# Kernel tuning notes

Measured on AMD Instinct MI355X. Metric: run time of the kernel, lower is better.

The kernel has to match this reference:

```python
import jax, jax.numpy as jnp
import numpy as np

N_NODES = 100000
N_EDGES = 3200000
D = 128


def setup_inputs() -> dict:
    key = jax.random.key(0)
    k1, k2, k3 = jax.random.split(key, 3)
    x = jax.random.normal(k1, (N_NODES, D), dtype=jnp.float32)
    edge_index = jax.random.randint(k2, (2, N_EDGES), 0, N_NODES, dtype=jnp.int64)
    W = jax.random.normal(k3, (D, D), dtype=jnp.float32) / np.sqrt(D)
    b = jnp.zeros((D,), dtype=jnp.float32)
    return {"x": x, "edge_index": edge_index, "W": W, "b": b}


def reference(x, edge_index, W, b):
    N = x.shape[0]
    # GCNConv: add self loops
    loop = jnp.arange(N, dtype=edge_index.dtype)
    src = jnp.concatenate([edge_index[0], loop])  # message source j
    dst = jnp.concatenate([edge_index[1], loop])  # aggregation target i
    # symmetric normalization: deg counted at targets (incl. self loops)
    deg = jax.ops.segment_sum(jnp.ones_like(dst, dtype=x.dtype), dst, num_segments=N)
    dinv = deg ** -0.5  # every node has deg >= 1 due to self loops
    norm = dinv[src] * dinv[dst]  # [E+N]
    # linear transform then gather-scale-scatter aggregation
    h = x @ W  # [N, D_out]
    msgs = h[src] * norm[:, None]  # [E+N, D_out]
    out = jax.ops.segment_sum(msgs, dst, num_segments=N) + b
    return jax.nn.relu(out)
```

## Files before the change

kernel.cpp:

```cpp
#include <hip/hip_runtime.h>

#define NN 100000
#define NE 3200000
#define DD 128
#define NB 391
#define NCH 256
#define CHUNK (NE / NCH)


typedef __attribute__((ext_vector_type(8))) short bf16x8;
typedef __attribute__((ext_vector_type(4))) float f32x4;

__device__ inline unsigned bf16pair(float a, float b) {
    unsigned ua = __float_as_uint(a); ua = (ua + 0x7fffu + ((ua >> 16) & 1u)) >> 16;
    unsigned ub = __float_as_uint(b); ub = (ub + 0x7fffu + ((ub >> 16) & 1u)) >> 16;
    return ua | (ub << 16);
}
__device__ inline float bflo(unsigned u) { return __uint_as_float(u << 16); }
__device__ inline float bfhi(unsigned u) { return __uint_as_float(u & 0xffff0000u); }

__global__ __launch_bounds__(256) void k_hist1(const int* __restrict__ dst, int* __restrict__ H,
                                               const float* __restrict__ W, unsigned* __restrict__ Wimg) {
    if (blockIdx.x < 32) {
        int i = blockIdx.x * 256 + threadIdx.x;
        int c = i >> 6, k2 = i & 63;
        unsigned v = bf16pair(W[(size_t)(k2 * 2) * DD + c], W[(size_t)(k2 * 2 + 1) * DD + c]);
        int byte = c * 256 + ((k2 * 4) ^ ((c & 7) << 4));
        *(unsigned*)((char*)Wimg + byte) = v;
    }
    __shared__ int h[NB];
    for (int i = threadIdx.x; i < NB; i += 256) h[i] = 0;
    __syncthreads();
    const int base = blockIdx.x * CHUNK;
    for (int i = threadIdx.x; i < CHUNK; i += 256)
        atomicAdd(&h[dst[base + i] >> 8], 1);
    __syncthreads();
    for (int i = threadIdx.x; i < NB; i += 256) H[blockIdx.x * NB + i] = h[i];
}

__global__ __launch_bounds__(256) void k_offB1(int* __restrict__ H, int* __restrict__ BT) {
    __shared__ int s[256];
    const int b = blockIdx.x;
    const int t = threadIdx.x;
    int v = H[t * NB + b];
    s[t] = v;
    __syncthreads();
    for (int off = 1; off < 256; off <<= 1) {
        int u = (t >= off) ? s[t - off] : 0;
        __syncthreads();
        s[t] += u;
        __syncthreads();
    }
    H[t * NB + b] = s[t] - v;
    if (t == 255) BT[b] = s[255];
}

__global__ __launch_bounds__(512) void k_offB2(const int* __restrict__ BT, int* __restrict__ BB) {
    __shared__ int s[512];
    const int t = threadIdx.x;
    int v = (t < NB) ? BT[t] : 0;
    s[t] = v;
    __syncthreads();
    for (int off = 1; off < 512; off <<= 1) {
        int u = (t >= off) ? s[t - off] : 0;
        __syncthreads();
        s[t] += u;
        __syncthreads();
    }
    if (t < NB) BB[t] = s[t] - v;
}

__global__ __launch_bounds__(256) void k_part(const int* __restrict__ src, const int* __restrict__ dst,
                                              const int* __restrict__ H, const int* __restrict__ BB,
                                              unsigned* __restrict__ P) {
    __shared__ int cur[NB];
    for (int i = threadIdx.x; i < NB; i += 256)
        cur[i] = BB[i] + H[blockIdx.x * NB + i];
    __syncthreads();
    const int base = blockIdx.x * CHUNK;
    for (int i = threadIdx.x; i < CHUNK; i += 256) {
        int s = src[base + i];
        int d = dst[base + i];
        int p = atomicAdd(&cur[d >> 8], 1);
        P[p] = ((unsigned)s << 8) | (unsigned)(d & 255);
    }
}

__global__ __launch_bounds__(256) void k_bsort(const unsigned* __restrict__ P, const int* __restrict__ BB,
                                               const int* __restrict__ BT, int* __restrict__ esrc,
                                               int* __restrict__ cnt, int* __restrict__ start) {
    __shared__ int hist[256], red[256], sexcl[256], fil[256];
    const int b = blockIdx.x;
    const int base = BB[b];
    const int n = BT[b];
    const int t = threadIdx.x;
    hist[t] = 0;
    __syncthreads();
    for (int i = t; i < n; i += 256)
        atomicAdd(&hist[P[base + i] & 255u], 1);
    __syncthreads();
    int c = hist[t];
    red[t] = c;
    __syncthreads();
    for (int off = 1; off < 256; off <<= 1) {
        int u = (t >= off) ? red[t - off] : 0;
        __syncthreads();
        red[t] += u;
        __syncthreads();
    }
    int excl = red[t] - c;
    sexcl[t] = excl;
    fil[t] = 0;
    int node = (b << 8) + t;
    if (node < NN) { cnt[node] = c; start[node] = base + excl; }
    __syncthreads();
    for (int i = t; i < n; i += 256) {
        unsigned p = P[base + i];
        int dl = (int)(p & 255u);
        int pos = atomicAdd(&fil[dl], 1);
        esrc[base + sexcl[dl] + pos] = (int)(p >> 8);
    }
}

__global__ __launch_bounds__(256) void k_gemm_mfma(
    const float* __restrict__ x, const unsigned* __restrict__ Wimg,
    const int* __restrict__ cnt, unsigned* __restrict__ g) {
    __shared__ unsigned lds[12288];
    unsigned* Wl = lds;
    unsigned* Xl = lds + 8192;
    const int tid = threadIdx.x;
    {
        const uint4* s4 = (const uint4*)Wimg;
        uint4* d4 = (uint4*)Wl;
        for (int i = tid; i < 2048; i += 256) d4[i] = s4[i];
    }
    const int row0 = blockIdx.x * 64;
    {
        int r = tid >> 2;
        int cchunk = tid & 3;
        int srow = row0 + r; if (srow > NN - 1) srow = NN - 1;
        const float4* xr = (const float4*)(x + (size_t)srow * DD + cchunk * 32);
#pragma unroll
        for (int i = 0; i < 4; ++i) {
            float4 f0 = xr[i * 2], f1 = xr[i * 2 + 1];
            uint4 wv;
            wv.x = bf16pair(f0.x, f0.y); wv.y = bf16pair(f0.z, f0.w);
            wv.z = bf16pair(f1.x, f1.y); wv.w = bf16pair(f1.z, f1.w);
            int byte = r * 256 + (((cchunk * 64) + i * 16) ^ ((r & 7) << 4));
            *(uint4*)((char*)Xl + byte) = wv;
        }
    }
    __syncthreads();
    const int w = tid >> 6;
    const int l = tid & 63;
    const int lr = l & 15, lk = l >> 4;
    bf16x8 a[4];
    {
        int r = w * 16 + lr;
#pragma unroll
        for (int kk = 0; kk < 4; ++kk) {
            int byte = r * 256 + ((kk * 64 + lk * 16) ^ ((r & 7) << 4));
            a[kk] = *(bf16x8*)((char*)Xl + byte);
        }
    }
    f32x4 acc[8];
#pragma unroll
    for (int t = 0; t < 8; ++t) acc[t] = (f32x4){0.f, 0.f, 0.f, 0.f};
#pragma unroll
    for (int t = 0; t < 8; ++t) {
        int c = t * 16 + lr;
#pragma unroll
        for (int kk = 0; kk < 4; ++kk) {
            int byte = c * 256 + ((kk * 64 + lk * 16) ^ ((c & 7) << 4));
            bf16x8 bfr = *(bf16x8*)((char*)Wl + byte);
            acc[t] = __builtin_amdgcn_mfma_f32_16x16x32_bf16(a[kk], bfr, acc[t], 0, 0, 0);
        }
    }
#pragma unroll
    for (int j = 0; j < 4; ++j) {
        int row = row0 + w * 16 + lk * 4 + j;
        if (row < NN) {
            float dinv = rsqrtf((float)(cnt[row] + 1));
#pragma unroll
            for (int t = 0; t < 4; ++t) {
                unsigned v = bf16pair(acc[t][j] * dinv, acc[t + 4][j] * dinv);
                g[(size_t)row * 64 + t * 16 + lr] = v;
            }
        }
    }
}

__global__ __launch_bounds__(256) void k_aggregate(
    const unsigned* __restrict__ g, const int* __restrict__ esrc,
    const int* __restrict__ start, const int* __restrict__ cnt,
    const float* __restrict__ b, float* __restrict__ out) {
    int node = blockIdx.x * 4 + (threadIdx.x >> 6);
    if (node >= NN) return;
    int lane = threadIdx.x & 63;
    unsigned u0 = g[(unsigned)node * 64u + lane];
    float ax = bflo(u0), ay = bfhi(u0);
    const int base = start[node];
    const int n = cnt[node];
    const int* ep = esrc + base;
    int j = 0;
    for (; j + 16 <= n; j += 16) {
        int e[16];
#pragma unroll
        for (int u = 0; u < 16; ++u) e[u] = __builtin_nontemporal_load(&ep[j + u]);
        unsigned v[16];
#pragma unroll
        for (int u = 0; u < 16; ++u)
            v[u] = g[(unsigned)e[u] * 64u + lane];
#pragma unroll
        for (int u = 0; u < 16; ++u) { ax += bflo(v[u]); ay += bfhi(v[u]); }
    }
    for (; j + 4 <= n; j += 4) {
        unsigned v0 = g[(unsigned)__builtin_nontemporal_load(&ep[j + 0]) * 64u + lane];
        unsigned v1 = g[(unsigned)__builtin_nontemporal_load(&ep[j + 1]) * 64u + lane];
        unsigned v2 = g[(unsigned)__builtin_nontemporal_load(&ep[j + 2]) * 64u + lane];
        unsigned v3 = g[(unsigned)__builtin_nontemporal_load(&ep[j + 3]) * 64u + lane];
        ax += bflo(v0) + bflo(v1) + bflo(v2) + bflo(v3);
        ay += bfhi(v0) + bfhi(v1) + bfhi(v2) + bfhi(v3);
    }
    for (; j < n; ++j) {
        unsigned v = g[(unsigned)__builtin_nontemporal_load(&ep[j]) * 64u + lane];
        ax += bflo(v); ay += bfhi(v);
    }
    float dinv = rsqrtf((float)(n + 1));
    float bx = b[lane], by = b[lane + 64];
    float ox = fmaxf(fmaf(ax, dinv, bx), 0.f);
    float oy = fmaxf(fmaf(ay, dinv, by), 0.f);
    __builtin_nontemporal_store(ox, &out[(size_t)node * DD + lane]);
    __builtin_nontemporal_store(oy, &out[(size_t)node * DD + lane + 64]);
}

extern "C" void kernel_launch(void* const* d_in, const int* in_sizes, int n_in,
                              void* d_out, int out_size, void* d_ws, size_t ws_size,
                              hipStream_t stream) {
    const float* x = (const float*)d_in[0];
    const int* edge = (const int*)d_in[1];
    const float* W = (const float*)d_in[2];
    const float* b = (const float*)d_in[3];
    float* out = (float*)d_out;

    char* ws = (char*)d_ws;
    int* cnt      = (int*)(ws);
    int* start    = (int*)(ws + 400 * 1024);
    int* BT       = (int*)(ws + 800 * 1024);
    int* BB       = (int*)(ws + 804 * 1024);
    unsigned* Wim = (unsigned*)(ws + 832 * 1024);
    int* H        = (int*)(ws + (1 << 20));
    int* esrc     = (int*)(ws + (2 << 20));
    unsigned* P   = (unsigned*)(ws + (15ull << 20));
    unsigned* g   = (unsigned*)(ws + (15ull << 20));

    const int* src = edge;
    const int* dst = edge + NE;

    k_hist1<<<NCH, 256, 0, stream>>>(dst, H, W, Wim);
    k_offB1<<<NB, 256, 0, stream>>>(H, BT);
    k_offB2<<<1, 512, 0, stream>>>(BT, BB);
    k_part<<<NCH, 256, 0, stream>>>(src, dst, H, BB, P);
    k_bsort<<<NB, 256, 0, stream>>>(P, BB, BT, esrc, cnt, start);
    k_gemm_mfma<<<(NN + 63) / 64, 256, 0, stream>>>(x, Wim, cnt, g);
    k_aggregate<<<(NN + 3) / 4, 256, 0, stream>>>(g, esrc, start, cnt, b, out);
}
```

Before: 209.1 us.

## Stage bucket entries in LDS, load GEMM A-fragments directly, drop nontemporal edge loads

The bucket-sort kernel now caches each bucket's packed entries in shared memory (when they fit) so the second pass reads LDS instead of re-reading global memory. The GEMM kernel drops the X staging through LDS and loads A fragments straight from global into registers, processing 128 rows per block with two row groups sharing each W fragment read. The aggregation kernel switches edge index loads from nontemporal to normal cached loads. These changes cut global re-reads and LDS traffic, at the cost of more LDS in the sort kernel and more registers in the GEMM.

```diff
diff --git a/kernel.cpp b/kernel.cpp
--- a/kernel.cpp
+++ b/kernel.cpp
@@ -6,6 +6,7 @@
 #define NB 391
 #define NCH 256
 #define CHUNK (NE / NCH)
+#define PSTAGE 9216
 
 
 typedef __attribute__((ext_vector_type(8))) short bf16x8;
@@ -90,14 +91,19 @@
                                                const int* __restrict__ BT, int* __restrict__ esrc,
                                                int* __restrict__ cnt, int* __restrict__ start) {
     __shared__ int hist[256], red[256], sexcl[256], fil[256];
+    __shared__ unsigned Ps[PSTAGE];
     const int b = blockIdx.x;
     const int base = BB[b];
     const int n = BT[b];
     const int t = threadIdx.x;
+    const bool fits = (n <= PSTAGE);
     hist[t] = 0;
     __syncthreads();
-    for (int i = t; i < n; i += 256)
-        atomicAdd(&hist[P[base + i] & 255u], 1);
+    for (int i = t; i < n; i += 256) {
+        unsigned p = P[base + i];
+        if (fits) Ps[i] = p;
+        atomicAdd(&hist[p & 255u], 1);
+    }
     __syncthreads();
     int c = hist[t];
     red[t] = c;
@@ -115,7 +121,7 @@
     if (node < NN) { cnt[node] = c; start[node] = base + excl; }
     __syncthreads();
     for (int i = t; i < n; i += 256) {
-        unsigned p = P[base + i];
+        unsigned p = fits ? Ps[i] : P[base + i];
         int dl = (int)(p & 255u);
         int pos = atomicAdd(&fil[dl], 1);
         esrc[base + sexcl[dl] + pos] = (int)(p >> 8);
@@ -125,47 +131,39 @@
 __global__ __launch_bounds__(256) void k_gemm_mfma(
     const float* __restrict__ x, const unsigned* __restrict__ Wimg,
     const int* __restrict__ cnt, unsigned* __restrict__ g) {
-    __shared__ unsigned lds[12288];
-    unsigned* Wl = lds;
-    unsigned* Xl = lds + 8192;
+    __shared__ unsigned Wl[8192];
     const int tid = threadIdx.x;
     {
         const uint4* s4 = (const uint4*)Wimg;
         uint4* d4 = (uint4*)Wl;
         for (int i = tid; i < 2048; i += 256) d4[i] = s4[i];
     }
-    const int row0 = blockIdx.x * 64;
-    {
-        int r = tid >> 2;
-        int cchunk = tid & 3;
-        int srow = row0 + r; if (srow > NN - 1) srow = NN - 1;
-        const float4* xr = (const float4*)(x + (size_t)srow * DD + cchunk * 32);
-#pragma unroll
-        for (int i = 0; i < 4; ++i) {
-            float4 f0 = xr[i * 2], f1 = xr[i * 2 + 1];
+    const int row0 = blockIdx.x * 128;
+    const int w = tid >> 6;
+    const int l = tid & 63;
+    const int lr = l & 15, lk = l >> 4;
+    bf16x8 a[2][4];
+#pragma unroll
+    for (int rg = 0; rg < 2; ++rg) {
+        int r = row0 + w * 32 + rg * 16 + lr;
+        if (r > NN - 1) r = NN - 1;
+        const float* xr = x + (size_t)r * DD;
+#pragma unroll
+        for (int kk = 0; kk < 4; ++kk) {
+            float4 f0 = *(const float4*)(xr + kk * 32 + lk * 8);
+            float4 f1 = *(const float4*)(xr + kk * 32 + lk * 8 + 4);
             uint4 wv;
             wv.x = bf16pair(f0.x, f0.y); wv.y = bf16pair(f0.z, f0.w);
             wv.z = bf16pair(f1.x, f1.y); wv.w = bf16pair(f1.z, f1.w);
-            int byte = r * 256 + (((cchunk * 64) + i * 16) ^ ((r & 7) << 4));
-            *(uint4*)((char*)Xl + byte) = wv;
+            a[rg][kk] = *(bf16x8*)&wv;
         }
     }
     __syncthreads();
-    const int w = tid >> 6;
-    const int l = tid & 63;
-    const int lr = l & 15, lk = l >> 4;
-    bf16x8 a[4];
-    {
-        int r = w * 16 + lr;
-#pragma unroll
-        for (int kk = 0; kk < 4; ++kk) {
-            int byte = r * 256 + ((kk * 64 + lk * 16) ^ ((r & 7) << 4));
-            a[kk] = *(bf16x8*)((char*)Xl + byte);
-        }
-    }
-    f32x4 acc[8];
-#pragma unroll
-    for (int t = 0; t < 8; ++t) acc[t] = (f32x4){0.f, 0.f, 0.f, 0.f};
+    f32x4 acc[2][8];
+#pragma unroll
+    for (int rg = 0; rg < 2; ++rg)
+#pragma unroll
+        for (int t = 0; t < 8; ++t) acc[rg][t] = (f32x4){0.f, 0.f, 0.f, 0.f};
 #pragma unroll
     for (int t = 0; t < 8; ++t) {
         int c = t * 16 + lr;
@@ -173,17 +171,20 @@
         for (int kk = 0; kk < 4; ++kk) {
             int byte = c * 256 + ((kk * 64 + lk * 16) ^ ((c & 7) << 4));
             bf16x8 bfr = *(bf16x8*)((char*)Wl + byte);
-            acc[t] = __builtin_amdgcn_mfma_f32_16x16x32_bf16(a[kk], bfr, acc[t], 0, 0, 0);
+            acc[0][t] = __builtin_amdgcn_mfma_f32_16x16x32_bf16(a[0][kk], bfr, acc[0][t], 0, 0, 0);
+            acc[1][t] = __builtin_amdgcn_mfma_f32_16x16x32_bf16(a[1][kk], bfr, acc[1][t], 0, 0, 0);
         }
     }
 #pragma unroll
+    for (int rg = 0; rg < 2; ++rg)
+#pragma unroll
     for (int j = 0; j < 4; ++j) {
-        int row = row0 + w * 16 + lk * 4 + j;
+        int row = row0 + w * 32 + rg * 16 + lk * 4 + j;
         if (row < NN) {
             float dinv = rsqrtf((float)(cnt[row] + 1));
 #pragma unroll
             for (int t = 0; t < 4; ++t) {
-                unsigned v = bf16pair(acc[t][j] * dinv, acc[t + 4][j] * dinv);
+                unsigned v = bf16pair(acc[rg][t][j] * dinv, acc[rg][t + 4][j] * dinv);
                 g[(size_t)row * 64 + t * 16 + lr] = v;
             }
         }
@@ -204,26 +205,23 @@
     const int* ep = esrc + base;
     int j = 0;
     for (; j + 16 <= n; j += 16) {
-        int e[16];
-#pragma unroll
-        for (int u = 0; u < 16; ++u) e[u] = __builtin_nontemporal_load(&ep[j + u]);
         unsigned v[16];
 #pragma unroll
         for (int u = 0; u < 16; ++u)
-            v[u] = g[(unsigned)e[u] * 64u + lane];
+            v[u] = g[(unsigned)ep[j + u] * 64u + lane];
 #pragma unroll
         for (int u = 0; u < 16; ++u) { ax += bflo(v[u]); ay += bfhi(v[u]); }
     }
     for (; j + 4 <= n; j += 4) {
-        unsigned v0 = g[(unsigned)__builtin_nontemporal_load(&ep[j + 0]) * 64u + lane];
-        unsigned v1 = g[(unsigned)__builtin_nontemporal_load(&ep[j + 1]) * 64u + lane];
-        unsigned v2 = g[(unsigned)__builtin_nontemporal_load(&ep[j + 2]) * 64u + lane];
-        unsigned v3 = g[(unsigned)__builtin_nontemporal_load(&ep[j + 3]) * 64u + lane];
+        unsigned v0 = g[(unsigned)ep[j + 0] * 64u + lane];
+        unsigned v1 = g[(unsigned)ep[j + 1] * 64u + lane];
+        unsigned v2 = g[(unsigned)ep[j + 2] * 64u + lane];
+        unsigned v3 = g[(unsigned)ep[j + 3] * 64u + lane];
         ax += bflo(v0) + bflo(v1) + bflo(v2) + bflo(v3);
         ay += bfhi(v0) + bfhi(v1) + bfhi(v2) + bfhi(v3);
     }
     for (; j < n; ++j) {
-        unsigned v = g[(unsigned)__builtin_nontemporal_load(&ep[j]) * 64u + lane];
+        unsigned v = g[(unsigned)ep[j] * 64u + lane];
         ax += bflo(v); ay += bfhi(v);
     }
     float dinv = rsqrtf((float)(n + 1));
@@ -262,6 +260,6 @@
     k_offB2<<<1, 512, 0, stream>>>(BT, BB);
     k_part<<<NCH, 256, 0, stream>>>(src, dst, H, BB, P);
     k_bsort<<<NB, 256, 0, stream>>>(P, BB, BT, esrc, cnt, start);
-    k_gemm_mfma<<<(NN + 63) / 64, 256, 0, stream>>>(x, Wim, cnt, g);
+    k_gemm_mfma<<<(NN + 127) / 128, 256, 0, stream>>>(x, Wim, cnt, g);
     k_aggregate<<<(NN + 3) / 4, 256, 0, stream>>>(g, esrc, start, cnt, b, out);
 }
```

New measurement: 201.2 us. 3.8% less time.
